# Performance work log

Measured on AMD Instinct MI355X. Metric: run time of the kernel, lower is better.

The kernel has to match this reference:

```python
import jax, jax.numpy as jnp
import numpy as np

SOS = 28          # RNNTParam.SOS = num_labels - 1
NUM_EMBED = 28    # num_labels - 1
C = 320           # pred_hidden_size
L = 2             # pred_num_layers
U, N = 128, 512   # decode steps, batch


def setup_inputs() -> dict:
    key = jax.random.key(0)
    ks = jax.random.split(key, 8)
    s = 1.0 / np.sqrt(C).astype(np.float32)
    x = jax.random.randint(ks[0], (U, N), 0, 29)                       # labels incl. SOS=28
    h0 = jax.random.normal(ks[1], (L, N, C), jnp.float32)
    c0 = jax.random.normal(ks[2], (L, N, C), jnp.float32)
    embed_weight = jax.random.normal(ks[3], (NUM_EMBED, C), jnp.float32)
    w_ih = jax.random.uniform(ks[4], (L, 4 * C, C), jnp.float32, -s, s)
    w_hh = jax.random.uniform(ks[5], (L, 4 * C, C), jnp.float32, -s, s)
    b_ih = jax.random.uniform(ks[6], (L, 4 * C), jnp.float32, -s, s)
    b_hh = jax.random.uniform(ks[7], (L, 4 * C), jnp.float32, -s, s)
    return dict(x=x, h0=h0, c0=c0, embed_weight=embed_weight,
                w_ih=w_ih, w_hh=w_hh, b_ih=b_ih, b_hh=b_hh)


def _lstm_layer(xs, h0, c0, w_ih, w_hh, b_ih, b_hh):
    # xs: [U, N, C]; torch LSTM gate order: i, f, g, o
    bias = b_ih + b_hh                                   # [4C]
    gx = jnp.einsum('unc,gc->ung', xs, w_ih) + bias      # precompute input part

    def step(carry, gx_t):
        h, c = carry
        gates = gx_t + h @ w_hh.T                        # [N, 4C]
        i, f, g, o = jnp.split(gates, 4, axis=-1)
        i = jax.nn.sigmoid(i)
        f = jax.nn.sigmoid(f)
        g = jnp.tanh(g)
        o = jax.nn.sigmoid(o)
        c = f * c + i * g
        h = o * jnp.tanh(c)
        return (h, c), h

    (hT, cT), ys = jax.lax.scan(step, (h0, c0), gx)
    return ys, hT, cT


def reference(x, h0, c0, embed_weight, w_ih, w_hh, b_ih, b_hh):
    sos_mask = (x == SOS)                                # [U, N]
    idx = jnp.where(sos_mask, 0, x)
    g = embed_weight[idx]                                # [U, N, C]
    g = jnp.where(sos_mask[..., None], 0.0, g)

    hs, cs = [], []
    for layer in range(L):
        g, hT, cT = _lstm_layer(g, h0[layer], c0[layer],
                                w_ih[layer], w_hh[layer],
                                b_ih[layer], b_hh[layer])
        hs.append(hT)
        cs.append(cT)
    hg = jnp.stack(hs, axis=0)                           # [L, N, C]
    cg = jnp.stack(cs, axis=0)
    return g, (hg, cg)
```

## Files before the change

### kernel.cpp

```cpp
#include <hip/hip_runtime.h>
#include <stdint.h>


typedef short short8 __attribute__((ext_vector_type(8)));
typedef float f32x4 __attribute__((ext_vector_type(4)));
typedef unsigned long long u64t;

#define USTEPS 128
#define HSZ    (512*320)
#define GSTEP  (512*320)
#define HGOFF  (128*512*320)
#define CGOFF  (HGOFF + 2*512*320)
#define FLAGSTRIDE 16

__device__ __forceinline__ uint16_t f2bf(float f) {
  union { float f; uint32_t i; } v; v.f = f;
  uint32_t i = v.i;
  return (uint16_t)((i + 0x7fffu + ((i >> 16) & 1u)) >> 16);
}
__device__ __forceinline__ float rcp_(float x) { return __builtin_amdgcn_rcpf(x); }
__device__ __forceinline__ float sigm(float x) { return rcp_(1.0f + __expf(-x)); }
__device__ __forceinline__ float tanh_(float x) {
  float ax = fabsf(x);
  float e  = __expf(-2.0f * ax);
  float t  = (1.0f - e) * rcp_(1.0f + e);
  return x < 0.0f ? -t : t;
}
__device__ __forceinline__ uint4 cvt8(const float* s) {
  float4 a = ((const float4*)s)[0];
  float4 b = ((const float4*)s)[1];
  uint4 r;
  r.x = (uint32_t)f2bf(a.x) | ((uint32_t)f2bf(a.y) << 16);
  r.y = (uint32_t)f2bf(a.z) | ((uint32_t)f2bf(a.w) << 16);
  r.z = (uint32_t)f2bf(b.x) | ((uint32_t)f2bf(b.y) << 16);
  r.w = (uint32_t)f2bf(b.z) | ((uint32_t)f2bf(b.w) << 16);
  return r;
}
__device__ __forceinline__ short8 loadw8(const float* p) {
  float4 a = ((const float4*)p)[0];
  float4 b = ((const float4*)p)[1];
  short8 r;
  r[0] = (short)f2bf(a.x); r[1] = (short)f2bf(a.y);
  r[2] = (short)f2bf(a.z); r[3] = (short)f2bf(a.w);
  r[4] = (short)f2bf(b.x); r[5] = (short)f2bf(b.y);
  r[6] = (short)f2bf(b.z); r[7] = (short)f2bf(b.w);
  return r;
}

__device__ __forceinline__ u64t slowld64(const void* p) {
  return __hip_atomic_load((const u64t*)p, __ATOMIC_RELAXED,
                           __HIP_MEMORY_SCOPE_AGENT);
}
template<bool FAST>
__device__ __forceinline__ u64t exld64(const void* p) {
  if (FAST) {
    u64t r;
    asm volatile("global_load_dwordx2 %0, %1, off sc0" : "=v"(r) : "v"(p));
    return r;
  } else {
    return slowld64(p);
  }
}
template<bool FAST>
__device__ __forceinline__ void exst32(void* p, uint32_t v) {
  if (FAST) {
    asm volatile("global_store_dword %0, %1, off sc0" :: "v"(p), "v"(v) : "memory");
  } else {
    __hip_atomic_store((uint32_t*)p, v, __ATOMIC_RELAXED,
                       __HIP_MEMORY_SCOPE_AGENT);
  }
}
__device__ __forceinline__ void vm_drain() {
  asm volatile("s_waitcnt vmcnt(0)" ::: "memory");
}

#define PREP_G0   (29 * 1280)
#define PREP_B1   (PREP_G0 + 1280)
#define PREP_FL   (PREP_B1 + 8448)
#define PREP_HI   (PREP_FL + 2 * 512 * 40)
__global__ void prep_kernel(const float* __restrict__ embed,
                            const float* __restrict__ w_ih,
                            const float* __restrict__ b_ih,
                            const float* __restrict__ b_hh,
                            const float* __restrict__ h0,
                            float* __restrict__ G0p,
                            float* __restrict__ bias1p,
                            uint32_t* __restrict__ flags,
                            uint16_t* __restrict__ Hx0,
                            uint16_t* __restrict__ Hx1) {
  int tid = blockIdx.x * blockDim.x + threadIdx.x;
  if (tid < PREP_G0) {
    int v = tid / 1280, col = tid % 1280;
    int hg = col / 80, idx = col % 80;
    int k = idx >> 2, q = idx & 3;
    int r = q * 320 + hg * 20 + k;
    float acc = b_ih[r] + b_hh[r];
    if (v < 28) {
      const float4* e = (const float4*)(embed + (size_t)v * 320);
      const float4* w = (const float4*)(w_ih + (size_t)r * 320);
#pragma unroll 4
      for (int i = 0; i < 80; ++i) {
        float4 a = e[i], b = w[i];
        acc += a.x * b.x + a.y * b.y + a.z * b.z + a.w * b.w;
      }
    }
    G0p[tid] = acc;
  } else if (tid < PREP_B1) {
    int col = tid - PREP_G0;
    int hg = col / 80, idx = col % 80;
    int k = idx >> 2, q = idx & 3;
    int r = q * 320 + hg * 20 + k;
    bias1p[col] = b_ih[1280 + r] + b_hh[1280 + r];
  } else if (tid < PREP_FL) {
    flags[tid - PREP_B1] = 0;
  } else if (tid < PREP_HI) {
    int id = tid - PREP_FL;
    int layer = id / 20480;
    int rem = id - layer * 20480;
    int n = rem / 40, c = rem - n * 40;
    const float* src = h0 + (size_t)layer * HSZ + (size_t)n * 320 + c * 8;
    uint16_t* dst = (layer ? Hx1 : Hx0) + HSZ + (size_t)n * 320 + c * 8;
    *(uint4*)dst = cvt8(src);
  }
}

template<bool FAST>
__device__ __forceinline__ void run_loop(
    const int* __restrict__ x, const float* __restrict__ c0,
    const float* __restrict__ w_ih, const float* __restrict__ w_hh,
    const float* __restrict__ G0p, const float* __restrict__ bias1p,
    uint16_t* __restrict__ Hx0, uint16_t* __restrict__ Hx1,
    uint32_t* __restrict__ flags, float* __restrict__ out,
    uint16_t* Hl0, uint16_t* Hl1, float* gates0, float* gates1,
    int* ctr0, int* ctr1) {
  const int tid  = threadIdx.x;
  const int wave = tid >> 6;
  const int lane = tid & 63;
  const int quad = lane >> 4;
  const int lm   = lane & 15;
  const int blk  = blockIdx.x;
  const int bg = (blk & 7) * 2 + (blk >> 7);
  const int hg = (blk >> 3) & 15;

  short8 Bhh0[10], Bih1[10], Bhh1[10];
  {
    int ncol = wave * 16 + lm;
    int k = ncol >> 2, q = ncol & 3;
    int r = q * 320 + hg * 20 + k;
    const float* p0 = w_hh + (size_t)r * 320 + quad * 8;
    const float* p1 = w_hh + (size_t)(1280 + r) * 320 + quad * 8;
    const float* pi = w_ih + (size_t)(1280 + r) * 320 + quad * 8;
#pragma unroll
    for (int kk = 0; kk < 10; ++kk) {
      Bhh0[kk] = loadw8(p0 + kk * 32);
      Bhh1[kk] = loadw8(p1 + kk * 32);
      Bih1[kk] = loadw8(pi + kk * 32);
    }
  }
  const float bias1v = bias1p[hg * 80 + wave * 16 + lm];

  const int un  = tid / 10;
  const int ukp = tid - un * 10;
  const int n_g = bg * 32 + un;
  const int kc  = hg * 20 + ukp * 2;

  int smc[8], spc[8];
#pragma unroll
  for (int it = 0; it < 8; ++it) {
    int cid = tid + it * 320;
    int m = cid / 80;
    int c8 = cid - m * 80;
    int c16 = c8 >> 1, h = c8 & 1;
    int p16 = c16 + m; if (p16 >= 40) p16 -= 40;
    smc[it] = m * 320 + c8 * 4;
    spc[it] = m * 320 + p16 * 8 + h * 4;
  }
  const size_t gbase = (size_t)bg * 32 * 320;

  float c0s0 = c0[(size_t)n_g * 320 + kc];
  float c0s1 = c0[(size_t)n_g * 320 + kc + 1];
  float c1s0 = c0[(size_t)(512 + n_g) * 320 + kc];
  float c1s1 = c0[(size_t)(512 + n_g) * 320 + kc + 1];

  uint32_t* flags0  = flags;
  uint32_t* flags1  = flags + 256 * FLAGSTRIDE;
  uint32_t* myflag0 = flags0 + (size_t)(bg * 16 + hg) * FLAGSTRIDE;
  uint32_t* myflag1 = flags1 + (size_t)(bg * 16 + hg) * FLAGSTRIDE;

  {
    const uint16_t* s0b = Hx0 + HSZ + gbase;
    u64t r0[8];
#pragma unroll
    for (int it = 0; it < 8; ++it) r0[it] = slowld64(s0b + smc[it]);
    vm_drain();
#pragma unroll
    for (int it = 0; it < 8; ++it) *(u64t*)(Hl0 + spc[it]) = r0[it];
    __syncthreads();
  }

  float4 gxa, gxb;
  {
    const int v = x[n_g];
    const float* gx = G0p + (size_t)v * 1280 + hg * 80 + ukp * 8;
    gxa = ((const float4*)gx)[0];
    gxb = ((const float4*)gx)[1];
  }

#pragma unroll 1
  for (int t = 0; t <= USTEPS; ++t) {
    const bool do0 = (t < USTEPS);
    const bool do1 = (t >= 1);

    f32x4 ag00 = {0.f, 0.f, 0.f, 0.f}, ag01 = {0.f, 0.f, 0.f, 0.f};
    f32x4 ag10 = {bias1v, bias1v, bias1v, bias1v}, ag11 = ag10;
#pragma unroll
    for (int kk = 0; kk < 10; ++kk) {
      int cch = kk * 4 + quad;
      int p0a = cch + lm;      if (p0a >= 40) p0a -= 40;
      int p1a = cch + lm + 16; if (p1a >= 40) p1a -= 40;
      short8 a00 = *(const short8*)(Hl0 + lm * 320 + p0a * 8);
      short8 a01 = *(const short8*)(Hl0 + (lm + 16) * 320 + p1a * 8);
      if (do0) {
        ag00 = __builtin_amdgcn_mfma_f32_16x16x32_bf16(a00, Bhh0[kk], ag00, 0, 0, 0);
        ag01 = __builtin_amdgcn_mfma_f32_16x16x32_bf16(a01, Bhh0[kk], ag01, 0, 0, 0);
      }
      if (do1) {
        ag10 = __builtin_amdgcn_mfma_f32_16x16x32_bf16(a00, Bih1[kk], ag10, 0, 0, 0);
        ag11 = __builtin_amdgcn_mfma_f32_16x16x32_bf16(a01, Bih1[kk], ag11, 0, 0, 0);
      }
    }

    if (do1 && t >= 2 && tid < 16) {
      uint32_t* peer = flags1 + (size_t)(bg * 16 + tid) * FLAGSTRIDE;
      while (__hip_atomic_load(peer, __ATOMIC_RELAXED,
                               __HIP_MEMORY_SCOPE_AGENT) < (uint32_t)t) {
      }
    }
    __syncthreads();

    if (do1) {
      const uint16_t* s1b = Hx1 + (size_t)(t & 1) * HSZ + gbase;
      u64t r1[8];
      if (FAST && t == 1) {
#pragma unroll
        for (int it = 0; it < 8; ++it) r1[it] = slowld64(s1b + smc[it]);
      } else {
#pragma unroll
        for (int it = 0; it < 8; ++it) r1[it] = exld64<FAST>(s1b + smc[it]);
      }
      vm_drain();
#pragma unroll
      for (int it = 0; it < 8; ++it) *(u64t*)(Hl1 + spc[it]) = r1[it];
    }
    if (do0) {
#pragma unroll
      for (int r = 0; r < 4; ++r) {
        gates0[(quad * 4 + r) * 84 + wave * 16 + lm]      = ag00[r];
        gates0[(16 + quad * 4 + r) * 84 + wave * 16 + lm] = ag01[r];
      }
    }
    __syncthreads();

    if (do0) {
      const float* gp = gates0 + un * 84 + ukp * 8;
      float i0 = gp[0] + gxa.x, f0 = gp[1] + gxa.y, g0 = gp[2] + gxa.z, o0 = gp[3] + gxa.w;
      float i1 = gp[4] + gxb.x, f1 = gp[5] + gxb.y, g1 = gp[6] + gxb.z, o1 = gp[7] + gxb.w;
      c0s0 = sigm(f0) * c0s0 + sigm(i0) * tanh_(g0);
      c0s1 = sigm(f1) * c0s1 + sigm(i1) * tanh_(g1);
      float ha = sigm(o0) * tanh_(c0s0);
      float hb = sigm(o1) * tanh_(c0s1);
      uint32_t packed = (uint32_t)f2bf(ha) | ((uint32_t)f2bf(hb) << 16);
      exst32<FAST>(Hx0 + (size_t)(t & 1) * HSZ + (size_t)n_g * 320 + kc, packed);
      if (t == USTEPS - 1) {
        *(float2*)(out + HGOFF + (size_t)n_g * 320 + kc) = make_float2(ha, hb);
        *(float2*)(out + CGOFF + (size_t)n_g * 320 + kc) = make_float2(c0s0, c0s1);
      }
    }

    if (do1) {
#pragma unroll
      for (int kk = 0; kk < 10; ++kk) {
        int cch = kk * 4 + quad;
        int p0a = cch + lm;      if (p0a >= 40) p0a -= 40;
        int p1a = cch + lm + 16; if (p1a >= 40) p1a -= 40;
        short8 a10 = *(const short8*)(Hl1 + lm * 320 + p0a * 8);
        short8 a11 = *(const short8*)(Hl1 + (lm + 16) * 320 + p1a * 8);
        ag10 = __builtin_amdgcn_mfma_f32_16x16x32_bf16(a10, Bhh1[kk], ag10, 0, 0, 0);
        ag11 = __builtin_amdgcn_mfma_f32_16x16x32_bf16(a11, Bhh1[kk], ag11, 0, 0, 0);
      }
    }

    if (do0) {
      vm_drain();
      if (lane == 0) {
        int old = atomicAdd(ctr0, 1);
        if ((old % 5) == 4)
          __hip_atomic_store(myflag0, (uint32_t)(t + 1), __ATOMIC_RELAXED,
                             __HIP_MEMORY_SCOPE_AGENT);
      }
    }

    if (do1) {
#pragma unroll
      for (int r = 0; r < 4; ++r) {
        gates1[(quad * 4 + r) * 84 + wave * 16 + lm]      = ag10[r];
        gates1[(16 + quad * 4 + r) * 84 + wave * 16 + lm] = ag11[r];
      }
    }
    __syncthreads();

    if (do1) {
      const int u1 = t - 1;
      const float* gp = gates1 + un * 84 + ukp * 8;
      float i0 = gp[0], f0 = gp[1], g0 = gp[2], o0 = gp[3];
      float i1 = gp[4], f1 = gp[5], g1 = gp[6], o1 = gp[7];
      c1s0 = sigm(f0) * c1s0 + sigm(i0) * tanh_(g0);
      c1s1 = sigm(f1) * c1s1 + sigm(i1) * tanh_(g1);
      float ha = sigm(o0) * tanh_(c1s0);
      float hb = sigm(o1) * tanh_(c1s1);
      uint32_t packed = (uint32_t)f2bf(ha) | ((uint32_t)f2bf(hb) << 16);
      exst32<FAST>(Hx1 + (size_t)((t + 1) & 1) * HSZ + (size_t)n_g * 320 + kc, packed);
      vm_drain();
      if (lane == 0) {
        int old = atomicAdd(ctr1, 1);
        if ((old % 5) == 4)
          __hip_atomic_store(myflag1, (uint32_t)(t + 1), __ATOMIC_RELAXED,
                             __HIP_MEMORY_SCOPE_AGENT);
      }
      *(float2*)(out + (size_t)u1 * GSTEP + (size_t)n_g * 320 + kc) = make_float2(ha, hb);
      if (t == USTEPS) {
        *(float2*)(out + HGOFF + (size_t)(512 + n_g) * 320 + kc) = make_float2(ha, hb);
        *(float2*)(out + CGOFF + (size_t)(512 + n_g) * 320 + kc) = make_float2(c1s0, c1s1);
      }
    }

    if (t + 1 < USTEPS) {
      const int v = x[(t + 1) * 512 + n_g];
      const float* gx = G0p + (size_t)v * 1280 + hg * 80 + ukp * 8;
      gxa = ((const float4*)gx)[0];
      gxb = ((const float4*)gx)[1];
    }

    if (t < USTEPS) {
      if (tid < 16) {
        uint32_t* peer = flags0 + (size_t)(bg * 16 + tid) * FLAGSTRIDE;
        while (__hip_atomic_load(peer, __ATOMIC_RELAXED,
                                 __HIP_MEMORY_SCOPE_AGENT) < (uint32_t)(t + 1)) {
        }
      }
      __syncthreads();
      const uint16_t* s0b = Hx0 + (size_t)(t & 1) * HSZ + gbase;
      u64t r0[8];
#pragma unroll
      for (int it = 0; it < 8; ++it) r0[it] = exld64<FAST>(s0b + smc[it]);
      vm_drain();
#pragma unroll
      for (int it = 0; it < 8; ++it) *(u64t*)(Hl0 + spc[it]) = r0[it];
      __syncthreads();
    }
  }
}

__global__ void __launch_bounds__(320, 2)
rnnt_kernel(const int* __restrict__ x,
            const float* __restrict__ c0,
            const float* __restrict__ w_ih,
            const float* __restrict__ w_hh,
            const float* __restrict__ G0p,
            const float* __restrict__ bias1p,
            uint16_t* __restrict__ Hx0,
            uint16_t* __restrict__ Hx1,
            uint32_t* __restrict__ flags,
            float* __restrict__ out) {
  __shared__ __align__(16) uint16_t Hl0[32 * 320];
  __shared__ __align__(16) uint16_t Hl1[32 * 320];
  __shared__ __align__(16) float    gates0[32 * 84];
  __shared__ __align__(16) float    gates1[32 * 84];
  __shared__ int ctr0, ctr1;
  __shared__ uint32_t v0sh;

  const int tid = threadIdx.x;
  const int blk = blockIdx.x;
  const int bg = (blk & 7) * 2 + (blk >> 7);
  const int hg = (blk >> 3) & 15;

  const uint32_t xcc = (uint32_t)__builtin_amdgcn_s_getreg((3 << 11) | 20) & 0xffu;
  const uint32_t mine = 0x100u | xcc;
  uint32_t* xcdtab = flags + 8192;

  if (tid == 0) {
    ctr0 = 0; ctr1 = 0;
    __hip_atomic_store(&xcdtab[bg * 16 + hg], mine, __ATOMIC_RELAXED,
                       __HIP_MEMORY_SCOPE_AGENT);
  }
  uint32_t v = 0;
  if (tid < 256) {
    do {
      v = __hip_atomic_load(&xcdtab[tid], __ATOMIC_RELAXED,
                            __HIP_MEMORY_SCOPE_AGENT);
    } while (v == 0u);
    if (tid == 0) v0sh = v;
  }
  __syncthreads();
  const uint32_t v0 = v0sh;
  const int anydiff = __syncthreads_or((tid < 256) ? (int)(v != v0) : 0);
  const int anybad  = __syncthreads_or(
      (tid < 256 && (tid >> 4) == bg) ? (int)(v != mine) : 0);
  const bool fastok = (anydiff != 0) && (anybad == 0);

  if (fastok)
    run_loop<true>(x, c0, w_ih, w_hh, G0p, bias1p, Hx0, Hx1, flags, out,
                   Hl0, Hl1, gates0, gates1, &ctr0, &ctr1);
  else
    run_loop<false>(x, c0, w_ih, w_hh, G0p, bias1p, Hx0, Hx1, flags, out,
                    Hl0, Hl1, gates0, gates1, &ctr0, &ctr1);
}

extern "C" void kernel_launch(void* const* d_in, const int* in_sizes, int n_in,
                              void* d_out, int out_size, void* d_ws, size_t ws_size,
                              hipStream_t stream) {
  (void)in_sizes; (void)n_in; (void)out_size; (void)ws_size;
  const int*   x     = (const int*)d_in[0];
  const float* h0    = (const float*)d_in[1];
  const float* c0    = (const float*)d_in[2];
  const float* embed = (const float*)d_in[3];
  const float* w_ih  = (const float*)d_in[4];
  const float* w_hh  = (const float*)d_in[5];
  const float* b_ih  = (const float*)d_in[6];
  const float* b_hh  = (const float*)d_in[7];
  float* out = (float*)d_out;

  char* ws = (char*)d_ws;
  float*    G0p   = (float*)(ws);
  float*    b1p   = (float*)(ws + 148480);
  uint32_t* flags = (uint32_t*)(ws + 153600);
  uint16_t* Hx0   = (uint16_t*)(ws + 187392);
  uint16_t* Hx1   = (uint16_t*)(ws + 842752);

  hipLaunchKernelGGL(prep_kernel, dim3((PREP_HI + 255) / 256), dim3(256), 0,
                     stream, embed, w_ih, b_ih, b_hh, h0, G0p, b1p, flags,
                     Hx0, Hx1);

  void* args[] = { (void*)&x, (void*)&c0, (void*)&w_ih, (void*)&w_hh,
                   (void*)&G0p, (void*)&b1p, (void*)&Hx0, (void*)&Hx1,
                   (void*)&flags, (void*)&out };
  hipLaunchCooperativeKernel((const void*)rnnt_kernel, dim3(256), dim3(320),
                             args, 0, stream);
}
```

Baseline: 690.3 us.

## Split batch rows into two halves and pipeline both layers per half

Each block's 32 batch rows are now processed as two 16-row halves. Both LSTM layers are computed together for one half, and the halves signal readiness through separate flag sets, so peers can start loading half A of the hidden state while half B is still computing. The layer-1 hidden-state fetch is merged with the layer-0 fetch at the end of the step and split across the two flag waits, which removes a global sync and wait from the middle of the step. The per-thread elementwise work drops from two columns to one, with neighbour values exchanged by shuffle before the packed stores. The dependency ordering is more intricate, and layer-1 now reads its own previous state in the same phase as layer-0's new state, so correctness relies on the flag semantics still matching.

```diff
diff --git a/kernel.cpp b/kernel.cpp
--- a/kernel.cpp
+++ b/kernel.cpp
@@ -131,8 +131,9 @@
     const float* __restrict__ G0p, const float* __restrict__ bias1p,
     uint16_t* __restrict__ Hx0, uint16_t* __restrict__ Hx1,
     uint32_t* __restrict__ flags, float* __restrict__ out,
-    uint16_t* Hl0, uint16_t* Hl1, float* gates0, float* gates1,
-    int* ctr0, int* ctr1) {
+    uint16_t* Hl0, uint16_t* Hl1,
+    float* g0A, float* g1A, float* g0B, float* g1B,
+    int* ctrA, int* ctrB) {
   const int tid  = threadIdx.x;
   const int wave = tid >> 6;
   const int lane = tid & 63;
@@ -159,10 +160,12 @@
   }
   const float bias1v = bias1p[hg * 80 + wave * 16 + lm];
 
-  const int un  = tid / 10;
-  const int ukp = tid - un * 10;
-  const int n_g = bg * 32 + un;
-  const int kc  = hg * 20 + ukp * 2;
+  const int un2 = tid / 20;
+  const int uk  = tid - un2 * 20;
+  const int bA  = bg * 32 + un2;
+  const int bB  = bA + 16;
+  const int kc  = hg * 20 + uk;
+  const bool ukeven = (uk & 1) == 0;
 
   int smc[8], spc[8];
 #pragma unroll
@@ -177,15 +180,15 @@
   }
   const size_t gbase = (size_t)bg * 32 * 320;
 
-  float c0s0 = c0[(size_t)n_g * 320 + kc];
-  float c0s1 = c0[(size_t)n_g * 320 + kc + 1];
-  float c1s0 = c0[(size_t)(512 + n_g) * 320 + kc];
-  float c1s1 = c0[(size_t)(512 + n_g) * 320 + kc + 1];
-
-  uint32_t* flags0  = flags;
-  uint32_t* flags1  = flags + 256 * FLAGSTRIDE;
-  uint32_t* myflag0 = flags0 + (size_t)(bg * 16 + hg) * FLAGSTRIDE;
-  uint32_t* myflag1 = flags1 + (size_t)(bg * 16 + hg) * FLAGSTRIDE;
+  float cA0 = c0[(size_t)bA * 320 + kc];
+  float cA1 = c0[(size_t)(512 + bA) * 320 + kc];
+  float cB0 = c0[(size_t)bB * 320 + kc];
+  float cB1 = c0[(size_t)(512 + bB) * 320 + kc];
+
+  uint32_t* flagsA  = flags;
+  uint32_t* flagsB  = flags + 256 * FLAGSTRIDE;
+  uint32_t* myflagA = flagsA + (size_t)(bg * 16 + hg) * FLAGSTRIDE;
+  uint32_t* myflagB = flagsB + (size_t)(bg * 16 + hg) * FLAGSTRIDE;
 
   {
     const uint16_t* s0b = Hx0 + HSZ + gbase;
@@ -198,12 +201,12 @@
     __syncthreads();
   }
 
-  float4 gxa, gxb;
+  float4 gxA, gxB;
   {
-    const int v = x[n_g];
-    const float* gx = G0p + (size_t)v * 1280 + hg * 80 + ukp * 8;
-    gxa = ((const float4*)gx)[0];
-    gxb = ((const float4*)gx)[1];
+    const int vA = x[bA];
+    const int vB = x[bB];
+    gxA = *(const float4*)(G0p + (size_t)vA * 1280 + hg * 80 + uk * 4);
+    gxB = *(const float4*)(G0p + (size_t)vB * 1280 + hg * 80 + uk * 4);
   }
 
 #pragma unroll 1
@@ -211,152 +214,212 @@
     const bool do0 = (t < USTEPS);
     const bool do1 = (t >= 1);
 
-    f32x4 ag00 = {0.f, 0.f, 0.f, 0.f}, ag01 = {0.f, 0.f, 0.f, 0.f};
-    f32x4 ag10 = {bias1v, bias1v, bias1v, bias1v}, ag11 = ag10;
-#pragma unroll
-    for (int kk = 0; kk < 10; ++kk) {
-      int cch = kk * 4 + quad;
-      int p0a = cch + lm;      if (p0a >= 40) p0a -= 40;
-      int p1a = cch + lm + 16; if (p1a >= 40) p1a -= 40;
-      short8 a00 = *(const short8*)(Hl0 + lm * 320 + p0a * 8);
-      short8 a01 = *(const short8*)(Hl0 + (lm + 16) * 320 + p1a * 8);
-      if (do0) {
-        ag00 = __builtin_amdgcn_mfma_f32_16x16x32_bf16(a00, Bhh0[kk], ag00, 0, 0, 0);
-        ag01 = __builtin_amdgcn_mfma_f32_16x16x32_bf16(a01, Bhh0[kk], ag01, 0, 0, 0);
-      }
-      if (do1) {
-        ag10 = __builtin_amdgcn_mfma_f32_16x16x32_bf16(a00, Bih1[kk], ag10, 0, 0, 0);
-        ag11 = __builtin_amdgcn_mfma_f32_16x16x32_bf16(a01, Bih1[kk], ag11, 0, 0, 0);
-      }
-    }
-
-    if (do1 && t >= 2 && tid < 16) {
-      uint32_t* peer = flags1 + (size_t)(bg * 16 + tid) * FLAGSTRIDE;
-      while (__hip_atomic_load(peer, __ATOMIC_RELAXED,
-                               __HIP_MEMORY_SCOPE_AGENT) < (uint32_t)t) {
-      }
-    }
-    __syncthreads();
-
-    if (do1) {
-      const uint16_t* s1b = Hx1 + (size_t)(t & 1) * HSZ + gbase;
-      u64t r1[8];
-      if (FAST && t == 1) {
-#pragma unroll
-        for (int it = 0; it < 8; ++it) r1[it] = slowld64(s1b + smc[it]);
-      } else {
-#pragma unroll
-        for (int it = 0; it < 8; ++it) r1[it] = exld64<FAST>(s1b + smc[it]);
-      }
-      vm_drain();
-#pragma unroll
-      for (int it = 0; it < 8; ++it) *(u64t*)(Hl1 + spc[it]) = r1[it];
-    }
-    if (do0) {
-#pragma unroll
-      for (int r = 0; r < 4; ++r) {
-        gates0[(quad * 4 + r) * 84 + wave * 16 + lm]      = ag00[r];
-        gates0[(16 + quad * 4 + r) * 84 + wave * 16 + lm] = ag01[r];
-      }
-    }
-    __syncthreads();
-
-    if (do0) {
-      const float* gp = gates0 + un * 84 + ukp * 8;
-      float i0 = gp[0] + gxa.x, f0 = gp[1] + gxa.y, g0 = gp[2] + gxa.z, o0 = gp[3] + gxa.w;
-      float i1 = gp[4] + gxb.x, f1 = gp[5] + gxb.y, g1 = gp[6] + gxb.z, o1 = gp[7] + gxb.w;
-      c0s0 = sigm(f0) * c0s0 + sigm(i0) * tanh_(g0);
-      c0s1 = sigm(f1) * c0s1 + sigm(i1) * tanh_(g1);
-      float ha = sigm(o0) * tanh_(c0s0);
-      float hb = sigm(o1) * tanh_(c0s1);
-      uint32_t packed = (uint32_t)f2bf(ha) | ((uint32_t)f2bf(hb) << 16);
-      exst32<FAST>(Hx0 + (size_t)(t & 1) * HSZ + (size_t)n_g * 320 + kc, packed);
-      if (t == USTEPS - 1) {
-        *(float2*)(out + HGOFF + (size_t)n_g * 320 + kc) = make_float2(ha, hb);
-        *(float2*)(out + CGOFF + (size_t)n_g * 320 + kc) = make_float2(c0s0, c0s1);
-      }
-    }
-
-    if (do1) {
+    {
+      f32x4 a0 = {0.f, 0.f, 0.f, 0.f};
+      f32x4 a1 = {bias1v, bias1v, bias1v, bias1v};
 #pragma unroll
       for (int kk = 0; kk < 10; ++kk) {
         int cch = kk * 4 + quad;
-        int p0a = cch + lm;      if (p0a >= 40) p0a -= 40;
-        int p1a = cch + lm + 16; if (p1a >= 40) p1a -= 40;
-        short8 a10 = *(const short8*)(Hl1 + lm * 320 + p0a * 8);
-        short8 a11 = *(const short8*)(Hl1 + (lm + 16) * 320 + p1a * 8);
-        ag10 = __builtin_amdgcn_mfma_f32_16x16x32_bf16(a10, Bhh1[kk], ag10, 0, 0, 0);
-        ag11 = __builtin_amdgcn_mfma_f32_16x16x32_bf16(a11, Bhh1[kk], ag11, 0, 0, 0);
-      }
-    }
-
-    if (do0) {
+        int p = cch + lm; if (p >= 40) p -= 40;
+        short8 h0f = *(const short8*)(Hl0 + lm * 320 + p * 8);
+        short8 h1f = *(const short8*)(Hl1 + lm * 320 + p * 8);
+        if (do0)
+          a0 = __builtin_amdgcn_mfma_f32_16x16x32_bf16(h0f, Bhh0[kk], a0, 0, 0, 0);
+        if (do1) {
+          a1 = __builtin_amdgcn_mfma_f32_16x16x32_bf16(h0f, Bih1[kk], a1, 0, 0, 0);
+          a1 = __builtin_amdgcn_mfma_f32_16x16x32_bf16(h1f, Bhh1[kk], a1, 0, 0, 0);
+        }
+      }
+#pragma unroll
+      for (int r = 0; r < 4; ++r) {
+        g0A[(quad * 4 + r) * 84 + wave * 16 + lm] = a0[r];
+        g1A[(quad * 4 + r) * 84 + wave * 16 + lm] = a1[r];
+      }
+    }
+    __syncthreads();
+
+    {
+      float4 g0 = *(const float4*)(g0A + un2 * 84 + uk * 4);
+      float4 g1 = *(const float4*)(g1A + un2 * 84 + uk * 4);
+      float h0v = 0.f, h1v = 0.f;
+      if (do0) {
+        float i = sigm(g0.x + gxA.x), f = sigm(g0.y + gxA.y);
+        float g = tanh_(g0.z + gxA.z), o = sigm(g0.w + gxA.w);
+        cA0 = f * cA0 + i * g;
+        h0v = o * tanh_(cA0);
+      }
+      if (do1) {
+        float i = sigm(g1.x), f = sigm(g1.y);
+        float g = tanh_(g1.z), o = sigm(g1.w);
+        cA1 = f * cA1 + i * g;
+        h1v = o * tanh_(cA1);
+      }
+      float h0p = __shfl_down(h0v, 1);
+      float h1p = __shfl_down(h1v, 1);
+      if (do0 && ukeven) {
+        uint32_t pk = (uint32_t)f2bf(h0v) | ((uint32_t)f2bf(h0p) << 16);
+        exst32<FAST>(Hx0 + (size_t)(t & 1) * HSZ + (size_t)bA * 320 + kc, pk);
+      }
+      if (do1 && ukeven) {
+        uint32_t pk = (uint32_t)f2bf(h1v) | ((uint32_t)f2bf(h1p) << 16);
+        exst32<FAST>(Hx1 + (size_t)((t + 1) & 1) * HSZ + (size_t)bA * 320 + kc, pk);
+      }
       vm_drain();
-      if (lane == 0) {
-        int old = atomicAdd(ctr0, 1);
+      if (t < USTEPS && lane == 0) {
+        int old = atomicAdd(ctrA, 1);
         if ((old % 5) == 4)
-          __hip_atomic_store(myflag0, (uint32_t)(t + 1), __ATOMIC_RELAXED,
+          __hip_atomic_store(myflagA, (uint32_t)(t + 1), __ATOMIC_RELAXED,
                              __HIP_MEMORY_SCOPE_AGENT);
       }
-    }
-
-    if (do1) {
+      if (do1 && ukeven)
+        *(float2*)(out + (size_t)(t - 1) * GSTEP + (size_t)bA * 320 + kc) =
+            make_float2(h1v, h1p);
+      float c0p = __shfl_down(cA0, 1);
+      float c1p = __shfl_down(cA1, 1);
+      if (do0 && t == USTEPS - 1 && ukeven) {
+        *(float2*)(out + HGOFF + (size_t)bA * 320 + kc) = make_float2(h0v, h0p);
+        *(float2*)(out + CGOFF + (size_t)bA * 320 + kc) = make_float2(cA0, c0p);
+      }
+      if (t == USTEPS && ukeven) {
+        *(float2*)(out + HGOFF + (size_t)(512 + bA) * 320 + kc) = make_float2(h1v, h1p);
+        *(float2*)(out + CGOFF + (size_t)(512 + bA) * 320 + kc) = make_float2(cA1, c1p);
+      }
+    }
+
+    {
+      f32x4 a0 = {0.f, 0.f, 0.f, 0.f};
+      f32x4 a1 = {bias1v, bias1v, bias1v, bias1v};
+#pragma unroll
+      for (int kk = 0; kk < 10; ++kk) {
+        int cch = kk * 4 + quad;
+        int p = cch + lm + 16; if (p >= 40) p -= 40;
+        short8 h0f = *(const short8*)(Hl0 + (lm + 16) * 320 + p * 8);
+        short8 h1f = *(const short8*)(Hl1 + (lm + 16) * 320 + p * 8);
+        if (do0)
+          a0 = __builtin_amdgcn_mfma_f32_16x16x32_bf16(h0f, Bhh0[kk], a0, 0, 0, 0);
+        if (do1) {
+          a1 = __builtin_amdgcn_mfma_f32_16x16x32_bf16(h0f, Bih1[kk], a1, 0, 0, 0);
+          a1 = __builtin_amdgcn_mfma_f32_16x16x32_bf16(h1f, Bhh1[kk], a1, 0, 0, 0);
+        }
+      }
 #pragma unroll
       for (int r = 0; r < 4; ++r) {
-        gates1[(quad * 4 + r) * 84 + wave * 16 + lm]      = ag10[r];
-        gates1[(16 + quad * 4 + r) * 84 + wave * 16 + lm] = ag11[r];
+        g0B[(quad * 4 + r) * 84 + wave * 16 + lm] = a0[r];
+        g1B[(quad * 4 + r) * 84 + wave * 16 + lm] = a1[r];
       }
     }
     __syncthreads();
 
-    if (do1) {
-      const int u1 = t - 1;
-      const float* gp = gates1 + un * 84 + ukp * 8;
-      float i0 = gp[0], f0 = gp[1], g0 = gp[2], o0 = gp[3];
-      float i1 = gp[4], f1 = gp[5], g1 = gp[6], o1 = gp[7];
-      c1s0 = sigm(f0) * c1s0 + sigm(i0) * tanh_(g0);
-      c1s1 = sigm(f1) * c1s1 + sigm(i1) * tanh_(g1);
-      float ha = sigm(o0) * tanh_(c1s0);
-      float hb = sigm(o1) * tanh_(c1s1);
-      uint32_t packed = (uint32_t)f2bf(ha) | ((uint32_t)f2bf(hb) << 16);
-      exst32<FAST>(Hx1 + (size_t)((t + 1) & 1) * HSZ + (size_t)n_g * 320 + kc, packed);
+    {
+      float4 g0 = *(const float4*)(g0B + un2 * 84 + uk * 4);
+      float4 g1 = *(const float4*)(g1B + un2 * 84 + uk * 4);
+      float h0v = 0.f, h1v = 0.f;
+      if (do0) {
+        float i = sigm(g0.x + gxB.x), f = sigm(g0.y + gxB.y);
+        float g = tanh_(g0.z + gxB.z), o = sigm(g0.w + gxB.w);
+        cB0 = f * cB0 + i * g;
+        h0v = o * tanh_(cB0);
+      }
+      if (do1) {
+        float i = sigm(g1.x), f = sigm(g1.y);
+        float g = tanh_(g1.z), o = sigm(g1.w);
+        cB1 = f * cB1 + i * g;
+        h1v = o * tanh_(cB1);
+      }
+      float h0p = __shfl_down(h0v, 1);
+      float h1p = __shfl_down(h1v, 1);
+      if (do0 && ukeven) {
+        uint32_t pk = (uint32_t)f2bf(h0v) | ((uint32_t)f2bf(h0p) << 16);
+        exst32<FAST>(Hx0 + (size_t)(t & 1) * HSZ + (size_t)bB * 320 + kc, pk);
+      }
+      if (do1 && ukeven) {
+        uint32_t pk = (uint32_t)f2bf(h1v) | ((uint32_t)f2bf(h1p) << 16);
+        exst32<FAST>(Hx1 + (size_t)((t + 1) & 1) * HSZ + (size_t)bB * 320 + kc, pk);
+      }
       vm_drain();
-      if (lane == 0) {
-        int old = atomicAdd(ctr1, 1);
+      if (t < USTEPS && lane == 0) {
+        int old = atomicAdd(ctrB, 1);
         if ((old % 5) == 4)
-          __hip_atomic_store(myflag1, (uint32_t)(t + 1), __ATOMIC_RELAXED,
+          __hip_atomic_store(myflagB, (uint32_t)(t + 1), __ATOMIC_RELAXED,
                              __HIP_MEMORY_SCOPE_AGENT);
       }
-      *(float2*)(out + (size_t)u1 * GSTEP + (size_t)n_g * 320 + kc) = make_float2(ha, hb);
-      if (t == USTEPS) {
-        *(float2*)(out + HGOFF + (size_t)(512 + n_g) * 320 + kc) = make_float2(ha, hb);
-        *(float2*)(out + CGOFF + (size_t)(512 + n_g) * 320 + kc) = make_float2(c1s0, c1s1);
+      if (do1 && ukeven)
+        *(float2*)(out + (size_t)(t - 1) * GSTEP + (size_t)bB * 320 + kc) =
+            make_float2(h1v, h1p);
+      float c0p = __shfl_down(cB0, 1);
+      float c1p = __shfl_down(cB1, 1);
+      if (do0 && t == USTEPS - 1 && ukeven) {
+        *(float2*)(out + HGOFF + (size_t)bB * 320 + kc) = make_float2(h0v, h0p);
+        *(float2*)(out + CGOFF + (size_t)bB * 320 + kc) = make_float2(cB0, c0p);
+      }
+      if (t == USTEPS && ukeven) {
+        *(float2*)(out + HGOFF + (size_t)(512 + bB) * 320 + kc) = make_float2(h1v, h1p);
+        *(float2*)(out + CGOFF + (size_t)(512 + bB) * 320 + kc) = make_float2(cB1, c1p);
       }
     }
 
     if (t + 1 < USTEPS) {
-      const int v = x[(t + 1) * 512 + n_g];
-      const float* gx = G0p + (size_t)v * 1280 + hg * 80 + ukp * 8;
-      gxa = ((const float4*)gx)[0];
-      gxb = ((const float4*)gx)[1];
+      const int vA = x[(t + 1) * 512 + bA];
+      const int vB = x[(t + 1) * 512 + bB];
+      gxA = *(const float4*)(G0p + (size_t)vA * 1280 + hg * 80 + uk * 4);
+      gxB = *(const float4*)(G0p + (size_t)vB * 1280 + hg * 80 + uk * 4);
     }
 
     if (t < USTEPS) {
       if (tid < 16) {
-        uint32_t* peer = flags0 + (size_t)(bg * 16 + tid) * FLAGSTRIDE;
+        uint32_t* peer = flagsA + (size_t)(bg * 16 + tid) * FLAGSTRIDE;
         while (__hip_atomic_load(peer, __ATOMIC_RELAXED,
                                  __HIP_MEMORY_SCOPE_AGENT) < (uint32_t)(t + 1)) {
         }
       }
       __syncthreads();
-      const uint16_t* s0b = Hx0 + (size_t)(t & 1) * HSZ + gbase;
-      u64t r0[8];
-#pragma unroll
-      for (int it = 0; it < 8; ++it) r0[it] = exld64<FAST>(s0b + smc[it]);
-      vm_drain();
-#pragma unroll
-      for (int it = 0; it < 8; ++it) *(u64t*)(Hl0 + spc[it]) = r0[it];
+      {
+        const uint16_t* s0b = Hx0 + (size_t)(t & 1) * HSZ + gbase;
+        const uint16_t* s1b = Hx1 + (size_t)((t + 1) & 1) * HSZ + gbase;
+        u64t r0[4], r1[4];
+#pragma unroll
+        for (int it = 0; it < 4; ++it) r0[it] = exld64<FAST>(s0b + smc[it]);
+        if (FAST && t == 0) {
+#pragma unroll
+          for (int it = 0; it < 4; ++it) r1[it] = slowld64(s1b + smc[it]);
+        } else {
+#pragma unroll
+          for (int it = 0; it < 4; ++it) r1[it] = exld64<FAST>(s1b + smc[it]);
+        }
+        vm_drain();
+#pragma unroll
+        for (int it = 0; it < 4; ++it) {
+          *(u64t*)(Hl0 + spc[it]) = r0[it];
+          *(u64t*)(Hl1 + spc[it]) = r1[it];
+        }
+      }
+      if (tid < 16) {
+        uint32_t* peer = flagsB + (size_t)(bg * 16 + tid) * FLAGSTRIDE;
+        while (__hip_atomic_load(peer, __ATOMIC_RELAXED,
+                                 __HIP_MEMORY_SCOPE_AGENT) < (uint32_t)(t + 1)) {
+        }
+      }
       __syncthreads();
+      {
+        const uint16_t* s0b = Hx0 + (size_t)(t & 1) * HSZ + gbase;
+        const uint16_t* s1b = Hx1 + (size_t)((t + 1) & 1) * HSZ + gbase;
+        u64t r0[4], r1[4];
+#pragma unroll
+        for (int it = 4; it < 8; ++it) r0[it - 4] = exld64<FAST>(s0b + smc[it]);
+        if (FAST && t == 0) {
+#pragma unroll
+          for (int it = 4; it < 8; ++it) r1[it - 4] = slowld64(s1b + smc[it]);
+        } else {
+#pragma unroll
+          for (int it = 4; it < 8; ++it) r1[it - 4] = exld64<FAST>(s1b + smc[it]);
+        }
+        vm_drain();
+#pragma unroll
+        for (int it = 4; it < 8; ++it) {
+          *(u64t*)(Hl0 + spc[it]) = r0[it - 4];
+          *(u64t*)(Hl1 + spc[it]) = r1[it - 4];
+        }
+      }
     }
   }
 }
@@ -374,9 +437,11 @@
             float* __restrict__ out) {
   __shared__ __align__(16) uint16_t Hl0[32 * 320];
   __shared__ __align__(16) uint16_t Hl1[32 * 320];
-  __shared__ __align__(16) float    gates0[32 * 84];
-  __shared__ __align__(16) float    gates1[32 * 84];
-  __shared__ int ctr0, ctr1;
+  __shared__ __align__(16) float    g0A[16 * 84];
+  __shared__ __align__(16) float    g1A[16 * 84];
+  __shared__ __align__(16) float    g0B[16 * 84];
+  __shared__ __align__(16) float    g1B[16 * 84];
+  __shared__ int ctrA, ctrB;
   __shared__ uint32_t v0sh;
 
   const int tid = threadIdx.x;
@@ -389,7 +454,7 @@
   uint32_t* xcdtab = flags + 8192;
 
   if (tid == 0) {
-    ctr0 = 0; ctr1 = 0;
+    ctrA = 0; ctrB = 0;
     __hip_atomic_store(&xcdtab[bg * 16 + hg], mine, __ATOMIC_RELAXED,
                        __HIP_MEMORY_SCOPE_AGENT);
   }
@@ -410,10 +475,10 @@
 
   if (fastok)
     run_loop<true>(x, c0, w_ih, w_hh, G0p, bias1p, Hx0, Hx1, flags, out,
-                   Hl0, Hl1, gates0, gates1, &ctr0, &ctr1);
+                   Hl0, Hl1, g0A, g1A, g0B, g1B, &ctrA, &ctrB);
   else
     run_loop<false>(x, c0, w_ih, w_hh, G0p, bias1p, Hx0, Hx1, flags, out,
-                    Hl0, Hl1, gates0, gates1, &ctr0, &ctr1);
+                    Hl0, Hl1, g0A, g1A, g0B, g1B, &ctrA, &ctrB);
 }
 
 extern "C" void kernel_launch(void* const* d_in, const int* in_sizes, int n_in,
```

Measured after the change: 769.1 us. 1.11x slower.
